# Kernel tuning notes

Measured on AMD Instinct MI355X. Metric: run time of the kernel, lower is better.

## Reference

```python
import jax, jax.numpy as jnp
import numpy as np

N_NODES = 100000
N_EDGES = 3200000
N_FEAT = 128
HIDDEN = 16


def gcn_conv(x, W, b, row, col, ew, n):
    """PyG GCNConv: linear -> add self-loops -> sym deg-norm -> scatter-add -> bias."""
    x = x @ W  # [n, out]
    loop = jnp.arange(n)
    row = jnp.concatenate([row, loop])
    col = jnp.concatenate([col, loop])
    ew = jnp.concatenate([ew, jnp.ones((n,), ew.dtype)])  # self-loop weight 1
    deg = jax.ops.segment_sum(ew, col, num_segments=n)  # in-degree by edge weight
    dinv = jnp.where(deg > 0, jax.lax.rsqrt(deg), 0.0)
    norm = dinv[row] * ew * dinv[col]  # [E+n]
    # gather source features, scale, scatter-add at destinations
    out = jax.ops.segment_sum(x[row] * norm[:, None], col, num_segments=n)
    return out + b


def setup_inputs() -> dict:
    key = jax.random.key(0)
    k = jax.random.split(key, 7)
    x = jax.random.normal(k[0], (N_NODES, N_FEAT), dtype=jnp.float32)
    edge_index = jax.random.randint(k[1], (2, N_EDGES), 0, N_NODES, dtype=jnp.int64)
    edge_weight = jax.random.uniform(k[2], (N_EDGES,), dtype=jnp.float32)
    s1 = 1.0 / np.sqrt(N_FEAT)
    s2 = 1.0 / np.sqrt(HIDDEN)
    W1 = jax.random.uniform(k[3], (N_FEAT, HIDDEN), jnp.float32, -s1, s1)
    b1 = jnp.zeros((HIDDEN,), jnp.float32)
    W2 = jax.random.uniform(k[4], (HIDDEN, 1), jnp.float32, -s2, s2)
    b2 = jnp.zeros((1,), jnp.float32)
    return {"x": x, "edge_index": edge_index, "edge_weight": edge_weight,
            "W1": W1, "b1": b1, "W2": W2, "b2": b2}


def reference(x, edge_index, edge_weight, W1, b1, W2, b2):
    n = x.shape[0]
    row, col = edge_index[0], edge_index[1]
    h = gcn_conv(x, W1, b1, row, col, edge_weight, n)
    h = jax.nn.relu(h)
    h = gcn_conv(h, W2, b2, row, col, edge_weight, n)
    return jax.nn.sigmoid(h)[:, 0].astype(jnp.float32)  # squeeze(1)
```

## Files before the change

kernel.cpp:

```cpp
#include <hip/hip_runtime.h>
#include <hip/hip_fp16.h>
#include <math.h>

#define NNODES 100000
#define NEDGES 3200000
#define NF 128
#define NH 16
#define SB 192
#define NSB 521
#define NBLK 512
#define EPB (NEDGES / NBLK)
#define CAP2 6912
#define XWBLK 391

__device__ __forceinline__ __half2 u2h(unsigned u) { union { unsigned u; __half2 h; } c; c.u = u; return c.h; }
__device__ __forceinline__ unsigned h2u(__half2 h) { union { unsigned u; __half2 h; } c; c.h = h; return c.u; }
__device__ __forceinline__ __half2 shfl_h2(__half2 v, int m) {
    int x = __shfl_xor(*(int*)&v, m);
    return *(__half2*)&x;
}

__global__ void k_histxw(const int* __restrict__ col, unsigned* __restrict__ ghist,
                         const float* __restrict__ x, const float* __restrict__ W1,
                         float* __restrict__ xw) {
    __shared__ float w[NF * NH];
    __shared__ unsigned h[NSB];
    int t = threadIdx.x, b = blockIdx.x;
    if (b < NBLK) {
        for (int i = t; i < NSB; i += 256) h[i] = 0u;
        __syncthreads();
        const int2* c2 = (const int2*)(col + b * EPB);
        for (int i = t; i < EPB / 2; i += 256) {
            int2 c = c2[i];
            atomicAdd(&h[(unsigned)c.x / SB], 1u);
            atomicAdd(&h[(unsigned)c.y / SB], 1u);
        }
        __syncthreads();
        for (int i = t; i < NSB; i += 256) ghist[(size_t)b * NSB + i] = h[i];
    } else {
        for (int i = t; i < NF * NH; i += 256) w[i] = W1[i];
        __syncthreads();
        int i = (b - NBLK) * 256 + t;
        if (i >= NNODES) return;
        float acc[NH];
#pragma unroll
        for (int f = 0; f < NH; ++f) acc[f] = 0.f;
        const float4* xr = (const float4*)(x + (long long)i * NF);
#pragma unroll 8
        for (int k4 = 0; k4 < NF / 4; ++k4) {
            float4 v = xr[k4];
            const float* wk = &w[k4 * 4 * NH];
#pragma unroll
            for (int f = 0; f < NH; ++f)
                acc[f] += v.x * wk[f] + v.y * wk[NH + f] + v.z * wk[2 * NH + f] + v.w * wk[3 * NH + f];
        }
        float4* o = (float4*)(xw + (size_t)i * NH);
#pragma unroll
        for (int q = 0; q < 4; ++q)
            o[q] = make_float4(acc[4 * q], acc[4 * q + 1], acc[4 * q + 2], acc[4 * q + 3]);
    }
}

__global__ __launch_bounds__(NBLK) void k_scan1(unsigned* __restrict__ ghist,
                                                unsigned* __restrict__ totals) {
    int k = blockIdx.x, t = threadIdx.x;
    __shared__ unsigned s[NBLK];
    unsigned v = ghist[(size_t)t * NSB + k];
    s[t] = v;
    __syncthreads();
    for (int off = 1; off < NBLK; off <<= 1) {
        unsigned x = (t >= off) ? s[t - off] : 0u;
        __syncthreads();
        s[t] += x;
        __syncthreads();
    }
    ghist[(size_t)t * NSB + k] = s[t] - v;
    if (t == NBLK - 1) totals[k] = s[t];
}

__global__ void k_scan2(const unsigned* __restrict__ totals, unsigned* __restrict__ sbase,
                        unsigned* __restrict__ start) {
    int t = threadIdx.x;
    __shared__ unsigned s[256];
    unsigned v[3];
    unsigned p = 0;
#pragma unroll
    for (int j = 0; j < 3; ++j) {
        int i = t * 3 + j;
        v[j] = (i < NSB) ? totals[i] : 0u;
        p += v[j];
    }
    s[t] = p;
    __syncthreads();
    for (int off = 1; off < 256; off <<= 1) {
        unsigned x = (t >= off) ? s[t - off] : 0u;
        __syncthreads();
        s[t] += x;
        __syncthreads();
    }
    unsigned run = s[t] - p;
#pragma unroll
    for (int j = 0; j < 3; ++j) {
        int i = t * 3 + j;
        if (i < NSB) sbase[i] = run;
        run += v[j];
    }
    if (t == 255) { sbase[NSB] = NEDGES; start[NNODES] = NEDGES; }
}

__global__ __launch_bounds__(256) void k_scatB1(
        const int* __restrict__ row, const int* __restrict__ col,
        const float* __restrict__ ew,
        const unsigned* __restrict__ ghist, const unsigned* __restrict__ sbase,
        uint2* __restrict__ spack) {
    __shared__ uint2 stage[EPB];
    __shared__ unsigned short sbArr[EPB];
    __shared__ unsigned lcnt[NSB];
    __shared__ unsigned gdelta[NSB];
    __shared__ unsigned scn[256];
    int t = threadIdx.x, b = blockIdx.x;
    int e0 = b * EPB;
    for (int i = t; i < NSB; i += 256) lcnt[i] = 0u;
    __syncthreads();
    const int2* c2 = (const int2*)(col + e0);
    for (int i = t; i < EPB / 2; i += 256) {
        int2 c = c2[i];
        atomicAdd(&lcnt[(unsigned)c.x / SB], 1u);
        atomicAdd(&lcnt[(unsigned)c.y / SB], 1u);
    }
    __syncthreads();
    unsigned v[3];
    unsigned p = 0;
#pragma unroll
    for (int j = 0; j < 3; ++j) {
        int i = t * 3 + j;
        v[j] = (i < NSB) ? lcnt[i] : 0u;
        p += v[j];
    }
    scn[t] = p;
    __syncthreads();
    for (int off = 1; off < 256; off <<= 1) {
        unsigned x = (t >= off) ? scn[t - off] : 0u;
        __syncthreads();
        scn[t] += x;
        __syncthreads();
    }
    unsigned run = scn[t] - p;
    __syncthreads();
    unsigned lst[3];
#pragma unroll
    for (int j = 0; j < 3; ++j) {
        int i = t * 3 + j;
        if (i < NSB) {
            lst[j] = run;
            gdelta[i] = sbase[i] + ghist[(size_t)b * NSB + i] - run;
        }
        run += v[j];
    }
    __syncthreads();
#pragma unroll
    for (int j = 0; j < 3; ++j) {
        int i = t * 3 + j;
        if (i < NSB) lcnt[i] = lst[j];
    }
    __syncthreads();
    const int2* r2 = (const int2*)(row + e0);
    const float2* w2 = (const float2*)(ew + e0);
    for (int i = t; i < EPB / 2; i += 256) {
        int2 rr = r2[i];
        int2 cc = c2[i];
        float2 ww = w2[i];
        unsigned sb = (unsigned)cc.x / SB;
        unsigned ln = (unsigned)cc.x - sb * SB;
        unsigned pos = atomicAdd(&lcnt[sb], 1u);
        stage[pos] = make_uint2((unsigned)rr.x | (ln << 17), __float_as_uint(ww.x));
        sbArr[pos] = (unsigned short)sb;
        sb = (unsigned)cc.y / SB;
        ln = (unsigned)cc.y - sb * SB;
        pos = atomicAdd(&lcnt[sb], 1u);
        stage[pos] = make_uint2((unsigned)rr.y | (ln << 17), __float_as_uint(ww.y));
        sbArr[pos] = (unsigned short)sb;
    }
    __syncthreads();
    for (int i = t; i < EPB; i += 256)
        spack[i + gdelta[sbArr[i]]] = stage[i];
}

__global__ __launch_bounds__(512) void k_degdinv(
        const uint2* __restrict__ spack, const unsigned* __restrict__ sbase,
        unsigned* __restrict__ start, float* __restrict__ dinv,
        const float* __restrict__ xw, unsigned* __restrict__ xwn) {
    __shared__ unsigned hist[SB];
    __shared__ float wdeg[SB];
    __shared__ unsigned scn[512];
    int k = blockIdx.x, t = threadIdx.x;
    unsigned e0 = sbase[k], e1 = sbase[k + 1];
    int ne = (int)(e1 - e0);
    if (t < SB) { hist[t] = 0u; wdeg[t] = 0.f; }
    __syncthreads();
    for (int i = t; i < ne; i += 512) {
        uint2 p = spack[e0 + i];
        unsigned ln = p.x >> 17;
        atomicAdd(&hist[ln], 1u);
        atomicAdd(&wdeg[ln], __uint_as_float(p.y));
    }
    __syncthreads();
    unsigned v = (t < SB) ? hist[t] : 0u;
    scn[t] = v;
    __syncthreads();
    for (int off = 1; off < 512; off <<= 1) {
        unsigned x = (t >= off) ? scn[t - off] : 0u;
        __syncthreads();
        scn[t] += x;
        __syncthreads();
    }
    unsigned excl = scn[t] - v;
    int g = k * SB + t;
    if (t < SB && g < NNODES) {
        start[g] = e0 + excl;
        float di = rsqrtf(wdeg[t] + 1.0f);
        dinv[g] = di;
        const float4* xr = (const float4*)(xw + (size_t)g * NH);
        float4 A = xr[0], B = xr[1], C = xr[2], D = xr[3];
        uint4 o0, o1;
        o0.x = h2u(__floats2half2_rn(A.x * di, A.y * di));
        o0.y = h2u(__floats2half2_rn(A.z * di, A.w * di));
        o0.z = h2u(__floats2half2_rn(B.x * di, B.y * di));
        o0.w = h2u(__floats2half2_rn(B.z * di, B.w * di));
        o1.x = h2u(__floats2half2_rn(C.x * di, C.y * di));
        o1.y = h2u(__floats2half2_rn(C.z * di, C.w * di));
        o1.z = h2u(__floats2half2_rn(D.x * di, D.y * di));
        o1.w = h2u(__floats2half2_rn(D.z * di, D.w * di));
        uint4* o = (uint4*)(xwn + (size_t)g * 8);
        o[0] = o0;
        o[1] = o1;
    }
}

__global__ __launch_bounds__(1024) void k_sedge1(
        uint2* __restrict__ spack, const unsigned* __restrict__ sbase,
        const unsigned* __restrict__ start, const unsigned* __restrict__ xwn,
        const float* __restrict__ dinv, const float* __restrict__ b1,
        const float* __restrict__ W2, float* __restrict__ zn) {
    __shared__ uint2 ed[CAP2];
    __shared__ unsigned lcnt[SB];
    int k = blockIdx.x, t = threadIdx.x;
    unsigned e0 = sbase[k], e1 = sbase[k + 1];
    int ne = (int)(e1 - e0);
    if (t < SB) {
        int g = k * SB + t;
        lcnt[t] = (g < NNODES) ? (start[g] - e0) : (unsigned)ne;
    }
    __syncthreads();
    for (int i = t; i < ne; i += 1024) {
        uint2 p = spack[e0 + i];
        unsigned ln = p.x >> 17;
        unsigned pos = atomicAdd(&lcnt[ln], 1u);
        __half2 hw = __float2half2_rn(__uint_as_float(p.y));
        ed[pos] = make_uint2(p.x & 0x1FFFFu, h2u(hw));
    }
    __syncthreads();
    for (int i = t; i < ne; i += 1024)
        spack[e0 + i] = ed[i];
    int wave = t >> 6, lane = t & 63;
    int fg = lane & 3, e4 = lane >> 2;
#pragma unroll
    for (int j = 0; j < SB / 16; ++j) {
        int ln = wave * (SB / 16) + j;
        int g = k * SB + ln;
        if (g >= NNODES) break;
        unsigned o0 = (ln == 0) ? 0u : lcnt[ln - 1];
        unsigned o1 = lcnt[ln];
        __half2 a0 = __float2half2_rn(0.f), a1 = a0;
        for (unsigned e = o0 + e4; e < o1; e += 16) {
            uint2 d = ed[e];
            uint2 q = *(const uint2*)(xwn + (size_t)d.x * 8 + fg * 2);
            a0 = __hfma2(u2h(q.x), u2h(d.y), a0);
            a1 = __hfma2(u2h(q.y), u2h(d.y), a1);
        }
#pragma unroll
        for (int m = 4; m < 64; m <<= 1) {
            a0 = __hadd2(a0, shfl_h2(a0, m));
            a1 = __hadd2(a1, shfl_h2(a1, m));
        }
        float ax = __low2float(a0), ay = __high2float(a0);
        float az = __low2float(a1), aw = __high2float(a1);
        uint2 qs = *(const uint2*)(xwn + (size_t)g * 8 + fg * 2);
        ax += __low2float(u2h(qs.x)); ay += __high2float(u2h(qs.x));
        az += __low2float(u2h(qs.y)); aw += __high2float(u2h(qs.y));
        float di = dinv[g];
        float4 b4 = ((const float4*)b1)[fg];
        float4 w4 = ((const float4*)W2)[fg];
        float s = fmaxf(di * ax + b4.x, 0.f) * w4.x
                + fmaxf(di * ay + b4.y, 0.f) * w4.y
                + fmaxf(di * az + b4.z, 0.f) * w4.z
                + fmaxf(di * aw + b4.w, 0.f) * w4.w;
        s += __shfl_xor(s, 1);
        s += __shfl_xor(s, 2);
        if (lane == 0) zn[g] = s * di;
    }
}

__global__ __launch_bounds__(256) void k_edge2out(
        const uint2* __restrict__ spack, const unsigned* __restrict__ start,
        const float* __restrict__ zn, const float* __restrict__ dinv,
        const float* __restrict__ b2, float* __restrict__ out) {
    int t = threadIdx.x;
    int n = blockIdx.x * 4 + (t >> 6);
    int lane = t & 63;
    unsigned e0 = start[n], e1 = start[n + 1];
    float acc = 0.f;
    for (unsigned e = e0 + lane; e < e1; e += 64) {
        uint2 p = spack[e];
        acc += zn[p.x] * __low2float(u2h(p.y));
    }
#pragma unroll
    for (int m = 1; m < 64; m <<= 1) acc += __shfl_xor(acc, m);
    if (lane == 0) {
        float di = dinv[n];
        float v = di * acc + di * zn[n] + b2[0];
        out[n] = 1.f / (1.f + expf(-v));
    }
}

extern "C" void kernel_launch(void* const* d_in, const int* in_sizes, int n_in,
                              void* d_out, int out_size, void* d_ws, size_t ws_size,
                              hipStream_t stream) {
    const float* x  = (const float*)d_in[0];
    const int* eidx = (const int*)d_in[1];
    const float* ew = (const float*)d_in[2];
    const float* W1 = (const float*)d_in[3];
    const float* b1 = (const float*)d_in[4];
    const float* W2 = (const float*)d_in[5];
    const float* b2 = (const float*)d_in[6];
    float* out = (float*)d_out;

    const int* row = eidx;
    const int* col = eidx + NEDGES;

    unsigned* ws = (unsigned*)d_ws;
    uint2*    spack  = (uint2*)ws;
    float*    xw     = (float*)(ws + 6400000);
    unsigned* xwn    = ws + 8000000;
    float*    dinv   = (float*)(ws + 8800000);
    float*    zn     = (float*)(ws + 8900000);
    unsigned* start  = ws + 9000000;
    unsigned* sbase  = ws + 9100001;
    unsigned* totals = ws + 9100523;
    unsigned* ghist  = ws + 9101044;

    k_histxw <<<NBLK + XWBLK, 256, 0, stream>>>(col, ghist, x, W1, xw);
    k_scan1  <<<NSB, NBLK, 0, stream>>>(ghist, totals);
    k_scan2  <<<1, 256, 0, stream>>>(totals, sbase, start);
    k_scatB1 <<<NBLK, 256, 0, stream>>>(row, col, ew, ghist, sbase, spack);
    k_degdinv<<<NSB, 512, 0, stream>>>(spack, sbase, start, dinv, xw, xwn);
    k_sedge1 <<<NSB, 1024, 0, stream>>>(spack, sbase, start, xwn, dinv, b1, W2, zn);
    k_edge2out<<<NNODES / 4, 256, 0, stream>>>(spack, start, zn, dinv, b2, out);
}
```

Before: 141.6 us.

## Fuse degree, layer-1 and layer-2 passes into one cooperative kernel

Merges the degree/dinv, layer-1 edge aggregation and layer-2 output kernels into a single cooperative launch that uses grid-wide syncs between phases. Each block keeps its sorted edges, offsets and dinv in shared memory across phases instead of writing start, dinv and a rewritten spack to global memory and reloading them. The node-bucket size changes to 200 so that 500 buckets exactly cover the nodes and the bounds checks can be dropped. In exchange it relies on all 500 blocks of 1024 threads being co-resident for the cooperative launch, and uses a larger shared-memory footprint per block.

Result: slower. 233.5 us (+64.8%).

```diff
diff --git a/kernel.cpp b/kernel.cpp
--- a/kernel.cpp
+++ b/kernel.cpp
@@ -1,16 +1,19 @@
 #include <hip/hip_runtime.h>
 #include <hip/hip_fp16.h>
+#include <hip/hip_cooperative_groups.h>
 #include <math.h>
+
+namespace cg = cooperative_groups;
 
 #define NNODES 100000
 #define NEDGES 3200000
 #define NF 128
 #define NH 16
-#define SB 192
-#define NSB 521
+#define SB 200
+#define NSB 500
 #define NBLK 512
 #define EPB (NEDGES / NBLK)
-#define CAP2 6912
+#define CAPF 7168
 #define XWBLK 391
 
 __device__ __forceinline__ __half2 u2h(unsigned u) { union { unsigned u; __half2 h; } c; c.u = u; return c.h; }
@@ -78,15 +81,14 @@
     if (t == NBLK - 1) totals[k] = s[t];
 }
 
-__global__ void k_scan2(const unsigned* __restrict__ totals, unsigned* __restrict__ sbase,
-                        unsigned* __restrict__ start) {
+__global__ void k_scan2(const unsigned* __restrict__ totals, unsigned* __restrict__ sbase) {
     int t = threadIdx.x;
     __shared__ unsigned s[256];
-    unsigned v[3];
+    unsigned v[2];
     unsigned p = 0;
 #pragma unroll
-    for (int j = 0; j < 3; ++j) {
-        int i = t * 3 + j;
+    for (int j = 0; j < 2; ++j) {
+        int i = t * 2 + j;
         v[j] = (i < NSB) ? totals[i] : 0u;
         p += v[j];
     }
@@ -100,12 +102,12 @@
     }
     unsigned run = s[t] - p;
 #pragma unroll
-    for (int j = 0; j < 3; ++j) {
-        int i = t * 3 + j;
+    for (int j = 0; j < 2; ++j) {
+        int i = t * 2 + j;
         if (i < NSB) sbase[i] = run;
         run += v[j];
     }
-    if (t == 255) { sbase[NSB] = NEDGES; start[NNODES] = NEDGES; }
+    if (t == 255) sbase[NSB] = NEDGES;
 }
 
 __global__ __launch_bounds__(256) void k_scatB1(
@@ -129,11 +131,11 @@
         atomicAdd(&lcnt[(unsigned)c.y / SB], 1u);
     }
     __syncthreads();
-    unsigned v[3];
+    unsigned v[2];
     unsigned p = 0;
 #pragma unroll
-    for (int j = 0; j < 3; ++j) {
-        int i = t * 3 + j;
+    for (int j = 0; j < 2; ++j) {
+        int i = t * 2 + j;
         v[j] = (i < NSB) ? lcnt[i] : 0u;
         p += v[j];
     }
@@ -147,10 +149,10 @@
     }
     unsigned run = scn[t] - p;
     __syncthreads();
-    unsigned lst[3];
-#pragma unroll
-    for (int j = 0; j < 3; ++j) {
-        int i = t * 3 + j;
+    unsigned lst[2];
+#pragma unroll
+    for (int j = 0; j < 2; ++j) {
+        int i = t * 2 + j;
         if (i < NSB) {
             lst[j] = run;
             gdelta[i] = sbase[i] + ghist[(size_t)b * NSB + i] - run;
@@ -159,8 +161,8 @@
     }
     __syncthreads();
 #pragma unroll
-    for (int j = 0; j < 3; ++j) {
-        int i = t * 3 + j;
+    for (int j = 0; j < 2; ++j) {
+        int i = t * 2 + j;
         if (i < NSB) lcnt[i] = lst[j];
     }
     __syncthreads();
@@ -186,19 +188,23 @@
         spack[i + gdelta[sbArr[i]]] = stage[i];
 }
 
-__global__ __launch_bounds__(512) void k_degdinv(
+__global__ __launch_bounds__(1024, 8) void k_fused(
         const uint2* __restrict__ spack, const unsigned* __restrict__ sbase,
-        unsigned* __restrict__ start, float* __restrict__ dinv,
-        const float* __restrict__ xw, unsigned* __restrict__ xwn) {
+        const float* __restrict__ xw, unsigned* __restrict__ xwn,
+        float* __restrict__ zn,
+        const float* __restrict__ b1, const float* __restrict__ W2,
+        const float* __restrict__ b2, float* __restrict__ out) {
+    __shared__ uint2 ed[CAPF];
     __shared__ unsigned hist[SB];
     __shared__ float wdeg[SB];
-    __shared__ unsigned scn[512];
+    __shared__ unsigned scn[1024];
+    cg::grid_group grid = cg::this_grid();
     int k = blockIdx.x, t = threadIdx.x;
     unsigned e0 = sbase[k], e1 = sbase[k + 1];
     int ne = (int)(e1 - e0);
     if (t < SB) { hist[t] = 0u; wdeg[t] = 0.f; }
     __syncthreads();
-    for (int i = t; i < ne; i += 512) {
+    for (int i = t; i < ne; i += 1024) {
         uint2 p = spack[e0 + i];
         unsigned ln = p.x >> 17;
         atomicAdd(&hist[ln], 1u);
@@ -208,18 +214,18 @@
     unsigned v = (t < SB) ? hist[t] : 0u;
     scn[t] = v;
     __syncthreads();
-    for (int off = 1; off < 512; off <<= 1) {
+    for (int off = 1; off < 1024; off <<= 1) {
         unsigned x = (t >= off) ? scn[t - off] : 0u;
         __syncthreads();
         scn[t] += x;
         __syncthreads();
     }
     unsigned excl = scn[t] - v;
-    int g = k * SB + t;
-    if (t < SB && g < NNODES) {
-        start[g] = e0 + excl;
+    if (t < SB) {
+        int g = k * SB + t;
         float di = rsqrtf(wdeg[t] + 1.0f);
-        dinv[g] = di;
+        wdeg[t] = di;
+        hist[t] = excl;
         const float4* xr = (const float4*)(xw + (size_t)g * NH);
         float4 A = xr[0], B = xr[1], C = xr[2], D = xr[3];
         uint4 o0, o1;
@@ -235,42 +241,21 @@
         o[0] = o0;
         o[1] = o1;
     }
-}
-
-__global__ __launch_bounds__(1024) void k_sedge1(
-        uint2* __restrict__ spack, const unsigned* __restrict__ sbase,
-        const unsigned* __restrict__ start, const unsigned* __restrict__ xwn,
-        const float* __restrict__ dinv, const float* __restrict__ b1,
-        const float* __restrict__ W2, float* __restrict__ zn) {
-    __shared__ uint2 ed[CAP2];
-    __shared__ unsigned lcnt[SB];
-    int k = blockIdx.x, t = threadIdx.x;
-    unsigned e0 = sbase[k], e1 = sbase[k + 1];
-    int ne = (int)(e1 - e0);
-    if (t < SB) {
-        int g = k * SB + t;
-        lcnt[t] = (g < NNODES) ? (start[g] - e0) : (unsigned)ne;
-    }
     __syncthreads();
     for (int i = t; i < ne; i += 1024) {
         uint2 p = spack[e0 + i];
         unsigned ln = p.x >> 17;
-        unsigned pos = atomicAdd(&lcnt[ln], 1u);
-        __half2 hw = __float2half2_rn(__uint_as_float(p.y));
-        ed[pos] = make_uint2(p.x & 0x1FFFFu, h2u(hw));
-    }
-    __syncthreads();
-    for (int i = t; i < ne; i += 1024)
-        spack[e0 + i] = ed[i];
+        unsigned pos = atomicAdd(&hist[ln], 1u);
+        ed[pos] = make_uint2(p.x & 0x1FFFFu, h2u(__float2half2_rn(__uint_as_float(p.y))));
+    }
+    __syncthreads();
+    grid.sync();
     int wave = t >> 6, lane = t & 63;
     int fg = lane & 3, e4 = lane >> 2;
-#pragma unroll
-    for (int j = 0; j < SB / 16; ++j) {
-        int ln = wave * (SB / 16) + j;
+    for (int ln = wave; ln < SB; ln += 16) {
         int g = k * SB + ln;
-        if (g >= NNODES) break;
-        unsigned o0 = (ln == 0) ? 0u : lcnt[ln - 1];
-        unsigned o1 = lcnt[ln];
+        unsigned o0 = (ln == 0) ? 0u : hist[ln - 1];
+        unsigned o1 = hist[ln];
         __half2 a0 = __float2half2_rn(0.f), a1 = a0;
         for (unsigned e = o0 + e4; e < o1; e += 16) {
             uint2 d = ed[e];
@@ -288,7 +273,7 @@
         uint2 qs = *(const uint2*)(xwn + (size_t)g * 8 + fg * 2);
         ax += __low2float(u2h(qs.x)); ay += __high2float(u2h(qs.x));
         az += __low2float(u2h(qs.y)); aw += __high2float(u2h(qs.y));
-        float di = dinv[g];
+        float di = wdeg[ln];
         float4 b4 = ((const float4*)b1)[fg];
         float4 w4 = ((const float4*)W2)[fg];
         float s = fmaxf(di * ax + b4.x, 0.f) * w4.x
@@ -299,27 +284,23 @@
         s += __shfl_xor(s, 2);
         if (lane == 0) zn[g] = s * di;
     }
-}
-
-__global__ __launch_bounds__(256) void k_edge2out(
-        const uint2* __restrict__ spack, const unsigned* __restrict__ start,
-        const float* __restrict__ zn, const float* __restrict__ dinv,
-        const float* __restrict__ b2, float* __restrict__ out) {
-    int t = threadIdx.x;
-    int n = blockIdx.x * 4 + (t >> 6);
-    int lane = t & 63;
-    unsigned e0 = start[n], e1 = start[n + 1];
-    float acc = 0.f;
-    for (unsigned e = e0 + lane; e < e1; e += 64) {
-        uint2 p = spack[e];
-        acc += zn[p.x] * __low2float(u2h(p.y));
-    }
-#pragma unroll
-    for (int m = 1; m < 64; m <<= 1) acc += __shfl_xor(acc, m);
-    if (lane == 0) {
-        float di = dinv[n];
-        float v = di * acc + di * zn[n] + b2[0];
-        out[n] = 1.f / (1.f + expf(-v));
+    grid.sync();
+    for (int ln = wave; ln < SB; ln += 16) {
+        int g = k * SB + ln;
+        unsigned o0 = (ln == 0) ? 0u : hist[ln - 1];
+        unsigned o1 = hist[ln];
+        float acc = 0.f;
+        for (unsigned e = o0 + lane; e < o1; e += 64) {
+            uint2 d = ed[e];
+            acc += zn[d.x] * __low2float(u2h(d.y));
+        }
+#pragma unroll
+        for (int m = 1; m < 64; m <<= 1) acc += __shfl_xor(acc, m);
+        if (lane == 0) {
+            float di = wdeg[ln];
+            float vv = di * acc + di * zn[g] + b2[0];
+            out[g] = 1.f / (1.f + expf(-vv));
+        }
     }
 }
 
@@ -342,18 +323,18 @@
     uint2*    spack  = (uint2*)ws;
     float*    xw     = (float*)(ws + 6400000);
     unsigned* xwn    = ws + 8000000;
-    float*    dinv   = (float*)(ws + 8800000);
-    float*    zn     = (float*)(ws + 8900000);
-    unsigned* start  = ws + 9000000;
-    unsigned* sbase  = ws + 9100001;
-    unsigned* totals = ws + 9100523;
-    unsigned* ghist  = ws + 9101044;
+    float*    zn     = (float*)(ws + 8800000);
+    unsigned* sbase  = ws + 8900000;
+    unsigned* totals = ws + 8900501;
+    unsigned* ghist  = ws + 8901001;
 
     k_histxw <<<NBLK + XWBLK, 256, 0, stream>>>(col, ghist, x, W1, xw);
     k_scan1  <<<NSB, NBLK, 0, stream>>>(ghist, totals);
-    k_scan2  <<<1, 256, 0, stream>>>(totals, sbase, start);
+    k_scan2  <<<1, 256, 0, stream>>>(totals, sbase);
     k_scatB1 <<<NBLK, 256, 0, stream>>>(row, col, ew, ghist, sbase, spack);
-    k_degdinv<<<NSB, 512, 0, stream>>>(spack, sbase, start, dinv, xw, xwn);
-    k_sedge1 <<<NSB, 1024, 0, stream>>>(spack, sbase, start, xwn, dinv, b1, W2, zn);
-    k_edge2out<<<NNODES / 4, 256, 0, stream>>>(spack, start, zn, dinv, b2, out);
-}
+
+    void* args[] = { (void*)&spack, (void*)&sbase, (void*)&xw, (void*)&xwn,
+                     (void*)&zn, (void*)&b1, (void*)&W2, (void*)&b2, (void*)&out };
+    hipLaunchCooperativeKernel((const void*)k_fused, dim3(NSB), dim3(1024),
+                               args, 0, stream);
+}
```

## Drop sorted edge write-back; aggregate layer-2 via shared-memory atomics per superblock

Applied to the files above, without the earlier changes.

The first edge kernel no longer writes its locally sorted, half-converted edge list back to global memory. Layer 2 now reads the unsorted superblock-packed edges directly and accumulates into a per-superblock shared array with atomics, keyed by the local node id in the high bits. This saves a full write pass over the edge array and swaps the 25k-block per-node reduction for 521 blocks. The cost is shared-memory atomic contention and far fewer blocks to keep the GPU busy.

Result: no change. 139.4 us (-1.6%).

```diff
diff --git a/kernel.cpp b/kernel.cpp
--- a/kernel.cpp
+++ b/kernel.cpp
@@ -238,7 +238,7 @@
 }
 
 __global__ __launch_bounds__(1024) void k_sedge1(
-        uint2* __restrict__ spack, const unsigned* __restrict__ sbase,
+        const uint2* __restrict__ spack, const unsigned* __restrict__ sbase,
         const unsigned* __restrict__ start, const unsigned* __restrict__ xwn,
         const float* __restrict__ dinv, const float* __restrict__ b1,
         const float* __restrict__ W2, float* __restrict__ zn) {
@@ -260,8 +260,6 @@
         ed[pos] = make_uint2(p.x & 0x1FFFFu, h2u(hw));
     }
     __syncthreads();
-    for (int i = t; i < ne; i += 1024)
-        spack[e0 + i] = ed[i];
     int wave = t >> 6, lane = t & 63;
     int fg = lane & 3, e4 = lane >> 2;
 #pragma unroll
@@ -301,25 +299,25 @@
     }
 }
 
-__global__ __launch_bounds__(256) void k_edge2out(
-        const uint2* __restrict__ spack, const unsigned* __restrict__ start,
+__global__ __launch_bounds__(512) void k_edge2acc(
+        const uint2* __restrict__ spack, const unsigned* __restrict__ sbase,
         const float* __restrict__ zn, const float* __restrict__ dinv,
         const float* __restrict__ b2, float* __restrict__ out) {
-    int t = threadIdx.x;
-    int n = blockIdx.x * 4 + (t >> 6);
-    int lane = t & 63;
-    unsigned e0 = start[n], e1 = start[n + 1];
-    float acc = 0.f;
-    for (unsigned e = e0 + lane; e < e1; e += 64) {
+    __shared__ float zacc[SB];
+    int k = blockIdx.x, t = threadIdx.x;
+    if (t < SB) zacc[t] = 0.f;
+    __syncthreads();
+    unsigned e0 = sbase[k], e1 = sbase[k + 1];
+    for (unsigned e = e0 + t; e < e1; e += 512) {
         uint2 p = spack[e];
-        acc += zn[p.x] * __low2float(u2h(p.y));
-    }
-#pragma unroll
-    for (int m = 1; m < 64; m <<= 1) acc += __shfl_xor(acc, m);
-    if (lane == 0) {
-        float di = dinv[n];
-        float v = di * acc + di * zn[n] + b2[0];
-        out[n] = 1.f / (1.f + expf(-v));
+        atomicAdd(&zacc[p.x >> 17], zn[p.x & 0x1FFFFu] * __uint_as_float(p.y));
+    }
+    __syncthreads();
+    int g = k * SB + t;
+    if (t < SB && g < NNODES) {
+        float di = dinv[g];
+        float v = di * zacc[t] + di * zn[g] + b2[0];
+        out[g] = 1.f / (1.f + expf(-v));
     }
 }
 
@@ -355,5 +353,5 @@
     k_scatB1 <<<NBLK, 256, 0, stream>>>(row, col, ew, ghist, sbase, spack);
     k_degdinv<<<NSB, 512, 0, stream>>>(spack, sbase, start, dinv, xw, xwn);
     k_sedge1 <<<NSB, 1024, 0, stream>>>(spack, sbase, start, xwn, dinv, b1, W2, zn);
-    k_edge2out<<<NNODES / 4, 256, 0, stream>>>(spack, start, zn, dinv, b2, out);
-}
+    k_edge2acc<<<NSB, 512, 0, stream>>>(spack, sbase, zn, dinv, b2, out);
+}
```
